# Kernel optimization log

Measured on AMD Instinct MI355X. Metric: run time of the kernel, lower is better.

Reference implementation:

```python
import jax, jax.numpy as jnp
import numpy as np
from jax import lax

EMBED = 64
FRAMES = 3
NNB = FRAMES - 1  # neighbor frames


def conv3x3(x, w, b):
    # x: [B,Cin,H,W], w: [Cout,Cin,3,3]
    y = lax.conv_general_dilated(x, w, (1, 1), [(1, 1), (1, 1)],
                                 dimension_numbers=("NCHW", "OIHW", "NCHW"))
    return y + b[None, :, None, None]


def setup_inputs() -> dict:
    key = jax.random.key(0)
    ks = jax.random.split(key, 9)
    s = lambda *sh: 1.0 / np.sqrt(np.prod(sh[1:]))
    return {
        "neighbor_frames": jax.random.normal(ks[0], (2, NNB, 96, 96), jnp.float32),
        "enc_w1": jax.random.normal(ks[1], (EMBED, 1, 3, 3), jnp.float32) * s(EMBED, 1, 3, 3),
        "enc_b1": jnp.zeros((EMBED,), jnp.float32),
        "enc_w2": jax.random.normal(ks[2], (EMBED, EMBED, 3, 3), jnp.float32) * s(EMBED, EMBED, 3, 3),
        "enc_b2": jnp.zeros((EMBED,), jnp.float32),
        "q_w": jax.random.normal(ks[3], (EMBED, NNB * EMBED), jnp.float32) * s(EMBED, NNB * EMBED),
        "q_b": jnp.zeros((EMBED,), jnp.float32),
        "k_w": jax.random.normal(ks[4], (EMBED, NNB * EMBED), jnp.float32) * s(EMBED, NNB * EMBED),
        "k_b": jnp.zeros((EMBED,), jnp.float32),
        "v_w": jax.random.normal(ks[5], (EMBED, NNB * EMBED), jnp.float32) * s(EMBED, NNB * EMBED),
        "v_b": jnp.zeros((EMBED,), jnp.float32),
    }


def reference(neighbor_frames, enc_w1, enc_b1, enc_w2, enc_b2,
              q_w, q_b, k_w, k_b, v_w, v_b):
    B, N, H, W = neighbor_frames.shape
    x = neighbor_frames.reshape(B * N, 1, H, W)
    # conv encoder (3x3 -> relu -> 3x3 -> relu)
    f = jax.nn.relu(conv3x3(x, enc_w1, enc_b1))
    f = jax.nn.relu(conv3x3(f, enc_w2, enc_b2))
    C = f.shape[1]
    # [B,N,C,H,W] -> [B, C*N? no: permute(0,2,1,3,4) -> B, C, N, H, W -> B, C*N, H, W]
    feat = f.reshape(B, N, C, H, W).transpose(0, 2, 1, 3, 4).reshape(B, C * N, H, W)
    # 1x1 qkv convs == per-pixel linear; flatten spatial to tokens t = H*W
    feat_t = feat.reshape(B, C * N, H * W)  # [B, Cin, T]
    Q = jnp.einsum("oc,bct->bot", q_w, feat_t) + q_b[None, :, None]
    K = jnp.einsum("oc,bct->bot", k_w, feat_t) + k_b[None, :, None]
    V = jnp.einsum("oc,bct->bot", v_w, feat_t) + v_b[None, :, None]
    scale = 1.0 / jnp.sqrt(jnp.asarray(Q.shape[1], Q.dtype))
    attn = jnp.einsum("bcn,bcm->bnm", Q, K) * scale  # [B, T, T]
    attn = jax.nn.softmax(attn, axis=-1)
    ctx = jnp.einsum("bnm,bcm->bcn", attn, V)  # [B, C, T]
    return ctx.reshape(B, C, H, W)
```

## Files before the change

### kernel.cpp

```cpp
#include <hip/hip_runtime.h>
#include <hip/hip_bf16.h>

#define TOK 9216
#define KSPLIT 5

typedef _Float16 half8 __attribute__((ext_vector_type(8)));
typedef float f32x4 __attribute__((ext_vector_type(4)));

#define GLOAD_LDS(g, l) \
    __builtin_amdgcn_global_load_lds((const __attribute__((address_space(1))) void*)(g), \
                                     (__attribute__((address_space(3))) void*)(l), 16, 0, 0)

#define QSCALE 0.18033688011112042f

#define OFF_F1   0u
#define SZ_F1    (4u*64u*TOK)
#define OFF_FEAT (OFF_F1 + SZ_F1)
#define SZ_FEAT  (2u*128u*TOK)
#define OFF_W1   (OFF_FEAT + SZ_FEAT + 3u*2u*64u*TOK)
#define OFF_B1   (OFF_W1 + 576u)
#define OFF_W2T  (OFF_B1 + 64u)
#define OFF_B2   (OFF_W2T + 36864u)
#define OFF_WCAT (OFF_B2 + 64u)
#define OFF_BCAT (OFF_WCAT + 24576u)

#define OFF_QT   4718592u
#define OFF_KT   5308416u
#define OFF_VH   5898240u

#define OFF_ML2  (OFF_FEAT + 9u*589824u)

__device__ __forceinline__ const float* part_base_c(const float* ws, int slab) {
    return ws + (slab < 8 ? (unsigned)slab * 589824u
                          : 6488064u + (unsigned)(slab - 8) * 589824u);
}
__device__ __forceinline__ float* part_base(float* ws, int slab) {
    return ws + (slab < 8 ? (unsigned)slab * 589824u
                          : 6488064u + (unsigned)(slab - 8) * 589824u);
}

__global__ __launch_bounds__(256) void conv1_kernel(
    const float* __restrict__ x,
    const float* __restrict__ w1, const float* __restrict__ b1,
    const float* __restrict__ w2, const float* __restrict__ b2,
    const float* __restrict__ qw, const float* __restrict__ qb,
    const float* __restrict__ kw, const float* __restrict__ kb,
    const float* __restrict__ vw, const float* __restrict__ vb,
    float* __restrict__ ws)
{
    int gid = blockIdx.x * 256 + threadIdx.x;

    if (gid < 64) ws[OFF_B2 + gid] = b2[gid];
    if (gid < 36864) {
        int co = gid / 576; int rem = gid % 576;
        int ci = rem / 9;  int tp = rem % 9;
        ((_Float16*)(ws + OFF_W2T))[co*576 + tp*64 + ci] = (_Float16)w2[gid];
    }
    if (gid < 24576) {
        int o = gid >> 7; int kidx = gid & 127;
        int n = kidx >> 6, c = kidx & 63;
        int sc = c*2 + n;
        float v;
        if (o < 64)       v = qw[o*128 + sc] * QSCALE;
        else if (o < 128) v = kw[(o-64)*128 + sc];
        else              v = vw[(o-128)*128 + sc];
        ((_Float16*)(ws + OFF_WCAT))[gid] = (_Float16)v;
    }
    if (gid < 192) {
        float v;
        if (gid < 64)       v = qb[gid] * QSCALE;
        else if (gid < 128) v = kb[gid-64];
        else                v = vb[gid-128];
        ws[OFF_BCAT + gid] = v;
    }

    _Float16* f1h = (_Float16*)(ws + OFF_F1);
    int px = gid >> 1, half = gid & 1;
    int img = px / TOK;
    int p   = px % TOK;
    int h = p / 96, w = p % 96;
    float xv[9];
    #pragma unroll
    for (int dh = 0; dh < 3; ++dh)
        #pragma unroll
        for (int dw = 0; dw < 3; ++dw) {
            int r = h + dh - 1, c = w + dw - 1;
            bool ok = (r >= 0) && (r < 96) && (c >= 0) && (c < 96);
            xv[dh*3 + dw] = ok ? x[img*TOK + r*96 + c] : 0.f;
        }
    _Float16* dst = f1h + (size_t)px * 64 + half * 32;
    #pragma unroll
    for (int g8 = 0; g8 < 4; ++g8) {
        union { _Float16 h[8]; uint4 u; } pk8;
        #pragma unroll
        for (int j = 0; j < 8; ++j) {
            int co = half*32 + g8*8 + j;
            float a = b1[co];
            #pragma unroll
            for (int t = 0; t < 9; ++t) a += w1[co*9 + t] * xv[t];
            pk8.h[j] = (_Float16)fmaxf(a, 0.f);
        }
        *(uint4*)&dst[g8*8] = pk8.u;
    }
}

__global__ __launch_bounds__(256) void conv2qkv_kernel(float* __restrict__ ws)
{
    __shared__ __align__(16) char fT[16384];

    int bid = blockIdx.x;
    int b   = bid / 144;
    int tile = bid % 144;
    int tid = threadIdx.x;
    int lane = tid & 63, w = tid >> 6;
    int lr = lane & 15, lk = lane >> 4;

    const _Float16* Wc  = (const _Float16*)(ws + OFF_W2T);
    const float* b2f = ws + OFF_B2;

    int t = tile*64 + w*16 + lr;
    int h = t / 96, wc = t % 96;

    half8 z8;
    #pragma unroll
    for (int i = 0; i < 8; ++i) z8[i] = (_Float16)0.f;

    #pragma unroll
    for (int n = 0; n < 2; ++n) {
        const _Float16* f1h = (const _Float16*)(ws + OFF_F1) + (size_t)(b*2 + n)*TOK*64;
        f32x4 acc[4];
        #pragma unroll
        for (int cs = 0; cs < 4; ++cs) {
            float bv = b2f[cs*16 + lr];
            acc[cs] = (f32x4){bv, bv, bv, bv};
        }
        #pragma unroll
        for (int ch = 0; ch < 18; ++ch) {
            int k = ch*32 + lk*8;
            int tap = k >> 6, ci = k & 63;
            int dh = tap / 3, dw = tap % 3;
            int r = h + dh - 1, c = wc + dw - 1;
            half8 af = z8;
            if ((unsigned)r < 96u && (unsigned)c < 96u)
                af = *(const half8*)&f1h[(size_t)(r*96 + c)*64 + ci];
            #pragma unroll
            for (int cs = 0; cs < 4; ++cs) {
                half8 bfr = *(const half8*)&Wc[(size_t)(cs*16 + lr)*576 + k];
                acc[cs] = __builtin_amdgcn_mfma_f32_16x16x32_f16(af, bfr, acc[cs], 0, 0, 0);
            }
        }
        #pragma unroll
        for (int cs = 0; cs < 4; ++cs)
            #pragma unroll
            for (int r = 0; r < 4; ++r) {
                int tl = w*16 + 4*lk + r;
                int off = tl*256 + (n*64 + cs*16 + lr)*2;
                *(_Float16*)(fT + (off ^ ((tl&7)<<4))) =
                    (_Float16)fmaxf(acc[cs][r], 0.f);
            }
    }
    __syncthreads();

    const _Float16* W  = (const _Float16*)(ws + OFF_WCAT);
    const float* bc = ws + OFF_BCAT;
    _Float16* QT = (_Float16*)(ws + OFF_QT) + (size_t)b*TOK*64;
    _Float16* KT = (_Float16*)(ws + OFF_KT) + (size_t)b*TOK*64;
    _Float16* VH = (_Float16*)(ws + OFF_VH) + (size_t)b*64*TOK;

    half8 bf[4][4];
    #pragma unroll
    for (int tt = 0; tt < 4; ++tt)
        #pragma unroll
        for (int kc = 0; kc < 4; ++kc) {
            int tl = tt*16 + lr;
            bf[tt][kc] = *(const half8*)(fT + ((tl*256 + kc*64 + lk*16) ^ ((tl&7)<<4)));
        }

    half8 af3[3][4];
    #pragma unroll
    for (int i = 0; i < 3; ++i)
        #pragma unroll
        for (int kc = 0; kc < 4; ++kc)
            af3[i][kc] = *(const half8*)&W[(size_t)((w*3 + i)*16 + lr)*128 + kc*32 + lk*8];

    #pragma unroll
    for (int i = 0; i < 3; ++i) {
        int ot = w*3 + i;
        f32x4 a[4];
        #pragma unroll
        for (int r = 0; r < 4; ++r) {
            float bv = bc[ot*16 + 4*lk + r];
            #pragma unroll
            for (int tt = 0; tt < 4; ++tt) a[tt][r] = bv;
        }
        #pragma unroll
        for (int kc = 0; kc < 4; ++kc)
            #pragma unroll
            for (int tt = 0; tt < 4; ++tt)
                a[tt] = __builtin_amdgcn_mfma_f32_16x16x32_f16(af3[i][kc], bf[tt][kc], a[tt], 0, 0, 0);
        #pragma unroll
        for (int tt = 0; tt < 4; ++tt) {
            int tg = tile*64 + tt*16 + lr;
            if (ot < 4) {
                union { _Float16 h[4]; uint2 u; } p;
                #pragma unroll
                for (int r = 0; r < 4; ++r) p.h[r] = (_Float16)a[tt][r];
                *(uint2*)&QT[(size_t)tg*64 + ot*16 + 4*lk] = p.u;
            } else if (ot < 8) {
                union { _Float16 h[4]; uint2 u; } p;
                #pragma unroll
                for (int r = 0; r < 4; ++r) p.h[r] = (_Float16)a[tt][r];
                *(uint2*)&KT[(size_t)tg*64 + (ot-4)*16 + 4*lk] = p.u;
            } else {
                #pragma unroll
                for (int r = 0; r < 4; ++r)
                    VH[(size_t)((ot-8)*16 + 4*lk + r)*TOK + tg] = (_Float16)a[tt][r];
            }
        }
    }
}

__global__ __launch_bounds__(512, 6) void attn_kernel(float* __restrict__ ws)
{
    __shared__ __align__(16) char smem[32768];
    float* ldsf = (float*)smem;

    int bid = blockIdx.x;
    int b   = bid / (72*KSPLIT);
    int rem = bid % (72*KSPLIT);
    int qt  = rem / KSPLIT;
    int ks  = rem % KSPLIT;
    int tid = threadIdx.x;
    int lane = tid & 63, w = tid >> 6;
    int wq = w & 3;
    int q0 = qt * 128;
    int lr = lane & 15;
    int lk = lane >> 4;

    int kb0 = (ks*144)/KSPLIT, kb1 = ((ks+1)*144)/KSPLIT;
    int nit = kb1 - kb0;
    int slab = b*KSPLIT + ks;

    const _Float16* Qt = (const _Float16*)(ws + OFF_QT) + (size_t)b*TOK*64;
    const _Float16* Kt = (const _Float16*)(ws + OFF_KT) + (size_t)b*TOK*64;
    const _Float16* Vh = (const _Float16*)(ws + OFF_VH) + (size_t)b*64*TOK;
    float* part = part_base(ws, slab);
    float* ml   = ws + OFF_ML2 + (size_t)slab*2*TOK;

    half8 qB[2];
    #pragma unroll
    for (int ch = 0; ch < 2; ++ch)
        qB[ch] = *(const half8*)&Qt[(size_t)(q0 + w*16 + lr)*64 + ch*32 + lk*8];

    const f32x4 Z4 = (f32x4){0.f, 0.f, 0.f, 0.f};
    half8 ones;
    #pragma unroll
    for (int i = 0; i < 8; ++i) ones[i] = (_Float16)1.0f;

    f32x4 O[4];
    #pragma unroll
    for (int cs = 0; cs < 4; ++cs) O[cs] = Z4;
    f32x4 lacc = Z4;
    float mM = -INFINITY;

    int segl = ((lane & 7) ^ ((lane >> 3) & 7)) * 8;
    int rrow = w*8 + (lane >> 3);
    unsigned kOff = (unsigned)(kb0*64 + rrow)*64u + (unsigned)segl;
    unsigned vOff = (unsigned)rrow*(unsigned)TOK + (unsigned)(kb0*64) + (unsigned)segl;
    unsigned wbase = (unsigned)(w * 1024);

    GLOAD_LDS(Kt + kOff, smem +         wbase);
    GLOAD_LDS(Vh + vOff, smem + 16384 + wbase);
    asm volatile("s_waitcnt vmcnt(0)" ::: "memory");
    __builtin_amdgcn_s_barrier();

    for (int it = 0; it < nit; ++it) {
        char* sKb = smem +         (it & 1) * 8192;
        char* sVb = smem + 16384 + (it & 1) * 8192;

        if (it + 1 < nit) {
            unsigned bufo = (unsigned)(((it + 1) & 1) * 8192) + wbase;
            GLOAD_LDS(Kt + kOff + (unsigned)(it + 1) * 4096u, smem + bufo);
            GLOAD_LDS(Vh + vOff + (unsigned)(it + 1) * 64u,   smem + 16384 + bufo);
        }

        f32x4 S[4];
        __builtin_amdgcn_s_setprio(1);
        #pragma unroll
        for (int st = 0; st < 4; ++st) {
            int t = st*16 + lr;
            half8 kA0 = *(const half8*)(sKb + ((t*128 +      lk*16) ^ ((t&7)<<4)));
            half8 kA1 = *(const half8*)(sKb + ((t*128 + 64 + lk*16) ^ ((t&7)<<4)));
            f32x4 s = __builtin_amdgcn_mfma_f32_16x16x32_f16(kA0, qB[0], Z4, 0, 0, 0);
            S[st]   = __builtin_amdgcn_mfma_f32_16x16x32_f16(kA1, qB[1], s,  0, 0, 0);
        }
        __builtin_amdgcn_s_setprio(0);

        float a0 = fmaxf(fmaxf(S[0][0], S[0][1]), S[0][2]);
        float a1 = fmaxf(fmaxf(S[0][3], S[1][0]), S[1][1]);
        float a2 = fmaxf(fmaxf(S[1][2], S[1][3]), S[2][0]);
        float a3 = fmaxf(fmaxf(S[2][1], S[2][2]), S[2][3]);
        float a4 = fmaxf(fmaxf(S[3][0], S[3][1]), S[3][2]);
        float pm = fmaxf(fmaxf(fmaxf(a0, a1), a2),
                         fmaxf(fmaxf(a3, a4), S[3][3]));
        pm = fmaxf(pm, __shfl_xor(pm, 16));
        pm = fmaxf(pm, __shfl_xor(pm, 32));

        if (__any(pm > mM + 8.0f)) {
            float mn = fmaxf(mM, pm);
            float fs = exp2f(mM - mn);
            mM = mn;
            #pragma unroll
            for (int cs = 0; cs < 4; ++cs)
                #pragma unroll
                for (int r = 0; r < 4; ++r) O[cs][r] *= fs;
            #pragma unroll
            for (int r = 0; r < 4; ++r) lacc[r] *= fs;
        }

        #pragma unroll
        for (int st = 0; st < 4; ++st)
            #pragma unroll
            for (int r = 0; r < 4; ++r)
                S[st][r] = exp2f(S[st][r] - mM);

        unsigned int pk2[4][2];
        #pragma unroll
        for (int st = 0; st < 4; ++st) {
            pk2[st][0] = __builtin_bit_cast(unsigned int,
                             __builtin_amdgcn_cvt_pkrtz(S[st][0], S[st][1]));
            pk2[st][1] = __builtin_bit_cast(unsigned int,
                             __builtin_amdgcn_cvt_pkrtz(S[st][2], S[st][3]));
        }

        int srcA = lr + 32*(lk & 1);
        int sel  = lk >> 1;
        __builtin_amdgcn_s_setprio(1);
        #pragma unroll
        for (int ch2 = 0; ch2 < 2; ++ch2) {
            union { unsigned int u[4]; half8 h; } pb;
            #pragma unroll
            for (int w2 = 0; w2 < 4; ++w2) {
                int src = srcA + 16*(w2 >> 1);
                int lo = __shfl((int)pk2[ch2*2 + 0][w2 & 1], src);
                int hi = __shfl((int)pk2[ch2*2 + 1][w2 & 1], src);
                pb.u[w2] = (unsigned int)(sel ? hi : lo);
            }
            lacc = __builtin_amdgcn_mfma_f32_16x16x32_f16(ones, pb.h, lacc, 0, 0, 0);
            #pragma unroll
            for (int cs = 0; cs < 4; ++cs) {
                int crow = cs*16 + lr;
                half8 vA = *(const half8*)(sVb + ((crow*128 + ch2*64 + lk*16) ^ ((crow&7)<<4)));
                O[cs] = __builtin_amdgcn_mfma_f32_16x16x32_f16(vA, pb.h, O[cs], 0, 0, 0);
            }
        }
        __builtin_amdgcn_s_setprio(0);

        asm volatile("s_waitcnt vmcnt(0)" ::: "memory");
        __builtin_amdgcn_s_barrier();
    }

    if (lk == 0) {
        ml[q0 + w*16 + lr]       = mM;
        ml[TOK + q0 + w*16 + lr] = lacc[0];
    }

    #pragma unroll
    for (int h = 0; h < 2; ++h) {
        if ((w >> 2) == h) {
            #pragma unroll
            for (int cs = 0; cs < 4; ++cs)
                #pragma unroll
                for (int r = 0; r < 4; ++r)
                    ldsf[(cs*16 + 4*lk + r)*68 + wq*16 + lr] = O[cs][r];
        }
        __syncthreads();
        int c = tid >> 3, qs = (tid & 7) * 8;
        const float* srcr = &ldsf[c*68 + qs];
        float* dstr = &part[(size_t)c*TOK + q0 + h*64 + qs];
        *(float4*)&dstr[0] = *(const float4*)&srcr[0];
        *(float4*)&dstr[4] = *(const float4*)&srcr[4];
        __syncthreads();
    }
}

__global__ __launch_bounds__(256) void recombine_kernel(
    const float* __restrict__ ws, float* __restrict__ out)
{
    int bid = blockIdx.x;
    int b   = bid / 144;
    int g2  = (bid % 144) * 256 + threadIdx.x;
    int cq  = g2 / 2304;
    int t   = (g2 % 2304) * 4;
    const float* mlp = ws + OFF_ML2;

    float4 m4[KSPLIT], l4[KSPLIT];
    float4 M = {-INFINITY, -INFINITY, -INFINITY, -INFINITY};
    #pragma unroll
    for (int ks = 0; ks < KSPLIT; ++ks) {
        int slab = b*KSPLIT + ks;
        m4[ks] = *(const float4*)&mlp[(size_t)slab*2*TOK + t];
        l4[ks] = *(const float4*)&mlp[(size_t)slab*2*TOK + TOK + t];
        M.x = fmaxf(M.x, m4[ks].x); M.y = fmaxf(M.y, m4[ks].y);
        M.z = fmaxf(M.z, m4[ks].z); M.w = fmaxf(M.w, m4[ks].w);
    }
    float4 wgt[KSPLIT];
    float4 den = {0.f, 0.f, 0.f, 0.f};
    #pragma unroll
    for (int ks = 0; ks < KSPLIT; ++ks) {
        wgt[ks].x = exp2f(m4[ks].x - M.x); wgt[ks].y = exp2f(m4[ks].y - M.y);
        wgt[ks].z = exp2f(m4[ks].z - M.z); wgt[ks].w = exp2f(m4[ks].w - M.w);
        den.x += l4[ks].x * wgt[ks].x; den.y += l4[ks].y * wgt[ks].y;
        den.z += l4[ks].z * wgt[ks].z; den.w += l4[ks].w * wgt[ks].w;
    }
    float4 inv = {1.f/den.x, 1.f/den.y, 1.f/den.z, 1.f/den.w};
    #pragma unroll
    for (int cc = 0; cc < 4; ++cc) {
        int c = cq*4 + cc;
        float4 acc = {0.f, 0.f, 0.f, 0.f};
        #pragma unroll
        for (int ks = 0; ks < KSPLIT; ++ks) {
            const float* part = part_base_c(ws, b*KSPLIT + ks);
            float4 p4 = *(const float4*)&part[(size_t)c*TOK + t];
            acc.x += p4.x * wgt[ks].x; acc.y += p4.y * wgt[ks].y;
            acc.z += p4.z * wgt[ks].z; acc.w += p4.w * wgt[ks].w;
        }
        float4 o4 = {acc.x*inv.x, acc.y*inv.y, acc.z*inv.z, acc.w*inv.w};
        *(float4*)&out[(size_t)(b*64 + c)*TOK + t] = o4;
    }
}

extern "C" void kernel_launch(void* const* d_in, const int* in_sizes, int n_in,
                              void* d_out, int out_size, void* d_ws, size_t ws_size,
                              hipStream_t stream)
{
    const float* frames = (const float*)d_in[0];
    const float* w1 = (const float*)d_in[1];
    const float* b1 = (const float*)d_in[2];
    const float* w2 = (const float*)d_in[3];
    const float* b2 = (const float*)d_in[4];
    const float* qw = (const float*)d_in[5];
    const float* qb = (const float*)d_in[6];
    const float* kw = (const float*)d_in[7];
    const float* kb = (const float*)d_in[8];
    const float* vw = (const float*)d_in[9];
    const float* vb = (const float*)d_in[10];
    float* ws = (float*)d_ws;
    float* out = (float*)d_out;

    hipLaunchKernelGGL(conv1_kernel, dim3(288), dim3(256), 0, stream,
                       frames, w1, b1, w2, b2, qw, qb, kw, kb, vw, vb, ws);
    hipLaunchKernelGGL(conv2qkv_kernel, dim3(288), dim3(256), 0, stream, ws);
    hipLaunchKernelGGL(attn_kernel, dim3(2*72*KSPLIT), dim3(512), 0, stream, ws);
    hipLaunchKernelGGL(recombine_kernel, dim3(288), dim3(256), 0, stream, ws, out);
}
```

Before: 156.9 us.

## Fuse split-K recombine into attention kernel via last-block atomic counter

Removes the separate recombine kernel launch. Each attention block increments a per-query-tile counter after a threadfence, and the last of the KSPLIT blocks merges the partial outputs and max/sum statistics and writes the final output. The counters are zeroed inside conv2qkv_kernel. This saves one launch and its drain gap, at the cost of atomics, fences and a serialized tail in the last-arriving block of each tile.

```diff
diff --git a/kernel.cpp b/kernel.cpp
--- a/kernel.cpp
+++ b/kernel.cpp
@@ -29,6 +29,7 @@
 #define OFF_VH   5898240u
 
 #define OFF_ML2  (OFF_FEAT + 9u*589824u)
+#define OFF_CNT  7852032u
 
 __device__ __forceinline__ const float* part_base_c(const float* ws, int slab) {
     return ws + (slab < 8 ? (unsigned)slab * 589824u
@@ -114,6 +115,8 @@
     int tid = threadIdx.x;
     int lane = tid & 63, w = tid >> 6;
     int lr = lane & 15, lk = lane >> 4;
+
+    if (bid == 0 && tid < 288) ((int*)(ws + OFF_CNT))[tid] = 0;
 
     const _Float16* Wc  = (const _Float16*)(ws + OFF_W2T);
     const float* b2f = ws + OFF_B2;
@@ -220,7 +223,8 @@
     }
 }
 
-__global__ __launch_bounds__(512, 6) void attn_kernel(float* __restrict__ ws)
+__global__ __launch_bounds__(512, 6) void attn_kernel(float* __restrict__ ws,
+                                                      float* __restrict__ out)
 {
     __shared__ __align__(16) char smem[32768];
     float* ldsf = (float*)smem;
@@ -382,51 +386,53 @@
         *(float4*)&dstr[4] = *(const float4*)&srcr[4];
         __syncthreads();
     }
-}
-
-__global__ __launch_bounds__(256) void recombine_kernel(
-    const float* __restrict__ ws, float* __restrict__ out)
-{
-    int bid = blockIdx.x;
-    int b   = bid / 144;
-    int g2  = (bid % 144) * 256 + threadIdx.x;
-    int cq  = g2 / 2304;
-    int t   = (g2 % 2304) * 4;
-    const float* mlp = ws + OFF_ML2;
-
-    float4 m4[KSPLIT], l4[KSPLIT];
-    float4 M = {-INFINITY, -INFINITY, -INFINITY, -INFINITY};
-    #pragma unroll
-    for (int ks = 0; ks < KSPLIT; ++ks) {
-        int slab = b*KSPLIT + ks;
-        m4[ks] = *(const float4*)&mlp[(size_t)slab*2*TOK + t];
-        l4[ks] = *(const float4*)&mlp[(size_t)slab*2*TOK + TOK + t];
-        M.x = fmaxf(M.x, m4[ks].x); M.y = fmaxf(M.y, m4[ks].y);
-        M.z = fmaxf(M.z, m4[ks].z); M.w = fmaxf(M.w, m4[ks].w);
-    }
-    float4 wgt[KSPLIT];
-    float4 den = {0.f, 0.f, 0.f, 0.f};
-    #pragma unroll
-    for (int ks = 0; ks < KSPLIT; ++ks) {
-        wgt[ks].x = exp2f(m4[ks].x - M.x); wgt[ks].y = exp2f(m4[ks].y - M.y);
-        wgt[ks].z = exp2f(m4[ks].z - M.z); wgt[ks].w = exp2f(m4[ks].w - M.w);
-        den.x += l4[ks].x * wgt[ks].x; den.y += l4[ks].y * wgt[ks].y;
-        den.z += l4[ks].z * wgt[ks].z; den.w += l4[ks].w * wgt[ks].w;
-    }
-    float4 inv = {1.f/den.x, 1.f/den.y, 1.f/den.z, 1.f/den.w};
-    #pragma unroll
-    for (int cc = 0; cc < 4; ++cc) {
-        int c = cq*4 + cc;
-        float4 acc = {0.f, 0.f, 0.f, 0.f};
-        #pragma unroll
-        for (int ks = 0; ks < KSPLIT; ++ks) {
-            const float* part = part_base_c(ws, b*KSPLIT + ks);
-            float4 p4 = *(const float4*)&part[(size_t)c*TOK + t];
-            acc.x += p4.x * wgt[ks].x; acc.y += p4.y * wgt[ks].y;
-            acc.z += p4.z * wgt[ks].z; acc.w += p4.w * wgt[ks].w;
-        }
-        float4 o4 = {acc.x*inv.x, acc.y*inv.y, acc.z*inv.z, acc.w*inv.w};
-        *(float4*)&out[(size_t)(b*64 + c)*TOK + t] = o4;
+
+    __threadfence();
+    __syncthreads();
+    volatile int* sOld = (volatile int*)smem;
+    if (tid == 0)
+        *sOld = atomicAdd((int*)(ws + OFF_CNT) + (b*72 + qt), 1);
+    __syncthreads();
+    if (*sOld == KSPLIT - 1) {
+        __threadfence();
+        const float* mlp = ws + OFF_ML2;
+        int t  = q0 + (tid & 31) * 4;
+        int cb = (tid >> 5) * 4;
+
+        float4 m4[KSPLIT], l4[KSPLIT];
+        float4 M = {-INFINITY, -INFINITY, -INFINITY, -INFINITY};
+        #pragma unroll
+        for (int s = 0; s < KSPLIT; ++s) {
+            int sl = b*KSPLIT + s;
+            m4[s] = *(const float4*)&mlp[(size_t)sl*2*TOK + t];
+            l4[s] = *(const float4*)&mlp[(size_t)sl*2*TOK + TOK + t];
+            M.x = fmaxf(M.x, m4[s].x); M.y = fmaxf(M.y, m4[s].y);
+            M.z = fmaxf(M.z, m4[s].z); M.w = fmaxf(M.w, m4[s].w);
+        }
+        float4 wgt[KSPLIT];
+        float4 den = {0.f, 0.f, 0.f, 0.f};
+        #pragma unroll
+        for (int s = 0; s < KSPLIT; ++s) {
+            wgt[s].x = exp2f(m4[s].x - M.x); wgt[s].y = exp2f(m4[s].y - M.y);
+            wgt[s].z = exp2f(m4[s].z - M.z); wgt[s].w = exp2f(m4[s].w - M.w);
+            den.x += l4[s].x * wgt[s].x; den.y += l4[s].y * wgt[s].y;
+            den.z += l4[s].z * wgt[s].z; den.w += l4[s].w * wgt[s].w;
+        }
+        float4 inv = {1.f/den.x, 1.f/den.y, 1.f/den.z, 1.f/den.w};
+        #pragma unroll
+        for (int cc = 0; cc < 4; ++cc) {
+            int c = cb + cc;
+            float4 acc = {0.f, 0.f, 0.f, 0.f};
+            #pragma unroll
+            for (int s = 0; s < KSPLIT; ++s) {
+                const float* pp = part_base_c(ws, b*KSPLIT + s);
+                float4 p4 = *(const float4*)&pp[(size_t)c*TOK + t];
+                acc.x += p4.x * wgt[s].x; acc.y += p4.y * wgt[s].y;
+                acc.z += p4.z * wgt[s].z; acc.w += p4.w * wgt[s].w;
+            }
+            float4 o4 = {acc.x*inv.x, acc.y*inv.y, acc.z*inv.z, acc.w*inv.w};
+            *(float4*)&out[(size_t)(b*64 + c)*TOK + t] = o4;
+        }
     }
 }
 
@@ -451,6 +457,5 @@
     hipLaunchKernelGGL(conv1_kernel, dim3(288), dim3(256), 0, stream,
                        frames, w1, b1, w2, b2, qw, qb, kw, kb, vw, vb, ws);
     hipLaunchKernelGGL(conv2qkv_kernel, dim3(288), dim3(256), 0, stream, ws);
-    hipLaunchKernelGGL(attn_kernel, dim3(2*72*KSPLIT), dim3(512), 0, stream, ws);
-    hipLaunchKernelGGL(recombine_kernel, dim3(288), dim3(256), 0, stream, ws, out);
-}
+    hipLaunchKernelGGL(attn_kernel, dim3(2*72*KSPLIT), dim3(512), 0, stream, ws, out);
+}
```

Result: slower. 399.7 us (+154.8%).
